# Kernel tuning notes

Hardware: AMD Instinct MI355X
Metric: run time of the kernel (lower is better)

The kernel has to match this reference:

```python
import jax, jax.numpy as jnp
import numpy as np

EMBED = 256
HEAD = 64
B, T = 16, 2048


def setup_inputs() -> dict:
    key = jax.random.key(0)
    kq, kk, kv, kwq, kwk, kwv = jax.random.split(key, 6)
    q = jax.random.normal(kq, (B, T, EMBED), dtype=jnp.float32)
    k = jax.random.normal(kk, (B, T, EMBED), dtype=jnp.float32)
    v = jax.random.normal(kv, (B, T, EMBED), dtype=jnp.float32)
    # causal mask matching the module's tril buffer semantics, broadcast over batch
    mask = jnp.tril(jnp.ones((T, T), dtype=jnp.int32))[None, :, :]
    s = 1.0 / np.sqrt(EMBED)
    Wq = (jax.random.normal(kwq, (EMBED, HEAD), dtype=jnp.float32) * s)
    Wk = (jax.random.normal(kwk, (EMBED, HEAD), dtype=jnp.float32) * s)
    Wv = (jax.random.normal(kwv, (EMBED, HEAD), dtype=jnp.float32) * s)
    return {"q": q, "k": k, "v": v, "mask": mask, "Wq": Wq, "Wk": Wk, "Wv": Wv}


def reference(q, k, v, mask, Wq, Wk, Wv):
    # projections (bias-free Linear): [B,T,E] @ [E,H] -> [B,T,H]
    C = k.shape[-1]
    qh = jnp.einsum('bte,eh->bth', q, Wq)
    kh = jnp.einsum('bte,eh->bth', k, Wk)
    vh = jnp.einsum('bte,eh->bth', v, Wv)
    # scores scaled by C**-0.5 (input embed dim, as in the source)
    wei = jnp.einsum('bth,bsh->bts', qh, kh) * (C ** -0.5)
    wei = jnp.where(mask == 0, -jnp.inf, wei)
    wei = jax.nn.softmax(wei, axis=-1)
    # dropout is identity in eval mode
    out = jnp.einsum('bts,bsh->bth', wei, vh)
    return out
```

## Files before the change

### kernel.cpp

```cpp
#include <hip/hip_runtime.h>
#include <hip/hip_bf16.h>
#include <cstdint>


#define NB 16
#define TT 2048
#define EE 256
#define HH 64

using bf16x8 = __attribute__((ext_vector_type(8))) __bf16;
using f32x4  = __attribute__((ext_vector_type(4))) float;
using u16x4  = __attribute__((ext_vector_type(4))) unsigned short;

static __device__ __forceinline__ unsigned short f2b(float f) {
  return __builtin_bit_cast(unsigned short, (__bf16)f);
}

__global__ __launch_bounds__(256) void prep_w_kernel(
    const float* __restrict__ Wq, const float* __restrict__ Wk,
    const float* __restrict__ Wv, unsigned short* __restrict__ wt) {
  int o = blockIdx.x * 256 + threadIdx.x;
  int p = o >> 14, rem = o & 16383;
  int n = rem >> 8, kk = rem & 255;
  const float* W = (p == 0) ? Wq : ((p == 1) ? Wk : Wv);
  float val = W[kk * HH + n];
  if (p == 0) val *= 0.09016844005555896f;
  wt[o] = f2b(val);
}

__global__ __launch_bounds__(256) void proj_kernel(
    const float* __restrict__ qi, const float* __restrict__ ki, const float* __restrict__ vi,
    const unsigned short* __restrict__ wt,
    unsigned short* __restrict__ qh, unsigned short* __restrict__ kh,
    unsigned short* __restrict__ vt) {
  const int p = blockIdx.y;
  const int row0 = blockIdx.x * 64;
  const float* __restrict__ src = (p == 0) ? qi : ((p == 1) ? ki : vi);
  const unsigned short* __restrict__ wp = wt + p * (HH * EE);

  __shared__ unsigned short A[64 * EE];
  const int tid = threadIdx.x;

  const float4* srcp = reinterpret_cast<const float4*>(src) + (size_t)row0 * (EE / 4);
  float4 f[16];
  #pragma unroll
  for (int i = 0; i < 16; ++i) f[i] = srcp[i * 256 + tid];
  #pragma unroll
  for (int i = 0; i < 16; ++i) {
    int c = i * 256 + tid;
    int r = c >> 6, d4 = c & 63;
    u16x4 h = { f2b(f[i].x), f2b(f[i].y), f2b(f[i].z), f2b(f[i].w) };
    int byte = r * 512 + ((d4 * 8) ^ ((r & 7) << 4));
    *reinterpret_cast<u16x4*>(reinterpret_cast<char*>(A) + byte) = h;
  }
  __syncthreads();

  const int wv = tid >> 6, lane = tid & 63, lr = lane & 15, lg = lane >> 4;
  f32x4 acc[4] = {};
  const int arow = wv * 16 + lr;
  const char* Abase = reinterpret_cast<const char*>(A) + arow * 512;
  #pragma unroll
  for (int k0 = 0; k0 < EE; k0 += 32) {
    bf16x8 af = *reinterpret_cast<const bf16x8*>(
        Abase + ((k0 * 2 + lg * 16) ^ ((arow & 7) << 4)));
    #pragma unroll
    for (int nt = 0; nt < 4; ++nt) {
      bf16x8 bfm = *reinterpret_cast<const bf16x8*>(wp + (nt * 16 + lr) * EE + k0 + lg * 8);
      acc[nt] = __builtin_amdgcn_mfma_f32_16x16x32_bf16(af, bfm, acc[nt], 0, 0, 0);
    }
  }

  if (p < 2) {
    unsigned short* dst = (p == 0) ? qh : kh;
    #pragma unroll
    for (int nt = 0; nt < 4; ++nt)
      #pragma unroll
      for (int r = 0; r < 4; ++r) {
        int grow = row0 + wv * 16 + lg * 4 + r;
        dst[(size_t)grow * HH + nt * 16 + lr] = f2b(acc[nt][r]);
      }
  } else {
    __syncthreads();
    #pragma unroll
    for (int nt = 0; nt < 4; ++nt)
      #pragma unroll
      for (int r = 0; r < 4; ++r) {
        int col = nt * 16 + lr;
        int trow = wv * 16 + lg * 4 + r;
        *reinterpret_cast<unsigned short*>(reinterpret_cast<char*>(A)
            + col * 128 + ((trow * 2) ^ ((col & 7) << 4))) = f2b(acc[nt][r]);
      }
    __syncthreads();
    const int bb = row0 >> 11, t0 = row0 & 2047;
    #pragma unroll
    for (int i = 0; i < 2; ++i) {
      int ch = i * 256 + tid;
      int col = ch >> 3, ro = (ch & 7) * 8;
      bf16x8 val = *reinterpret_cast<const bf16x8*>(reinterpret_cast<char*>(A)
          + col * 128 + ((ro * 2) ^ ((col & 7) << 4)));
      *reinterpret_cast<bf16x8*>(vt + (size_t)(bb * 64 + col) * TT + t0 + ro) = val;
    }
  }
}

__global__ __launch_bounds__(256) void attn_kernel(
    const unsigned short* __restrict__ qh, const unsigned short* __restrict__ kh,
    const unsigned short* __restrict__ vt, float* __restrict__ out) {
  __shared__ unsigned short K_lds[2][64 * 64];
  __shared__ unsigned short V_lds[2][64 * 64];
  __shared__ unsigned short P_lds[4][1024];

  const int tid = threadIdx.x;
  const int wv = tid >> 6, lane = tid & 63, lr = lane & 15, lg = lane >> 4;

  const int bid = blockIdx.x;
  const int half = bid >> 8, j = bid & 255;
  const int b = j >> 4;
  const int qt = half ? (31 - (j & 15)) : (j & 15);
  const int q0 = qt * 64;

  const unsigned short* qrow = qh + ((size_t)b * TT + q0 + wv * 16 + lr) * HH;
  bf16x8 qf0 = *reinterpret_cast<const bf16x8*>(qrow + lg * 8);
  bf16x8 qf1 = *reinterpret_cast<const bf16x8*>(qrow + 32 + lg * 8);

  const unsigned short* kb = kh + (size_t)b * TT * HH;
  const unsigned short* vb = vt + (size_t)b * HH * TT;
  char* pbase = reinterpret_cast<char*>(P_lds[wv]);

  const int rr0 = tid >> 3, of0 = (tid & 7) * 8;
  const int rr1 = (256 + tid) >> 3, of1 = (tid & 7) * 8;
  bf16x8 kr0, kr1, vr0, vr1;

#define LOADKV(kt_) do {                                                         \
    const unsigned short* kp_ = kb + (size_t)(kt_) * 64 * HH;                    \
    const unsigned short* vp_ = vb + (kt_) * 64;                                 \
    kr0 = *reinterpret_cast<const bf16x8*>(kp_ + rr0 * HH + of0);                \
    kr1 = *reinterpret_cast<const bf16x8*>(kp_ + rr1 * HH + of1);                \
    vr0 = *reinterpret_cast<const bf16x8*>(vp_ + (size_t)rr0 * TT + of0);        \
    vr1 = *reinterpret_cast<const bf16x8*>(vp_ + (size_t)rr1 * TT + of1);        \
  } while (0)

#define WRITEKV(bi_) do {                                                        \
    *reinterpret_cast<bf16x8*>(reinterpret_cast<char*>(K_lds[bi_])              \
        + rr0 * 128 + ((of0 * 2) ^ ((rr0 & 7) << 4))) = kr0;                     \
    *reinterpret_cast<bf16x8*>(reinterpret_cast<char*>(K_lds[bi_])              \
        + rr1 * 128 + ((of1 * 2) ^ ((rr1 & 7) << 4))) = kr1;                     \
    *reinterpret_cast<bf16x8*>(reinterpret_cast<char*>(V_lds[bi_])              \
        + rr0 * 128 + ((of0 * 2) ^ ((rr0 & 7) << 4))) = vr0;                     \
    *reinterpret_cast<bf16x8*>(reinterpret_cast<char*>(V_lds[bi_])              \
        + rr1 * 128 + ((of1 * 2) ^ ((rr1 & 7) << 4))) = vr1;                     \
  } while (0)

  f32x4 oa[4] = {};
  float ldacc[4] = {0.f, 0.f, 0.f, 0.f};

  LOADKV(0);
  WRITEKV(0);
  __syncthreads();

  for (int kt = 0; kt <= qt; ++kt) {
    const int cb = kt & 1;
    if (kt < qt) LOADKV(kt + 1);

    f32x4 s[4] = {};
    __builtin_amdgcn_s_setprio(1);
    #pragma unroll
    for (int ks = 0; ks < 2; ++ks)
      #pragma unroll
      for (int nt = 0; nt < 4; ++nt) {
        int key = nt * 16 + lr;
        bf16x8 kf = *reinterpret_cast<const bf16x8*>(
            reinterpret_cast<const char*>(K_lds[cb])
            + key * 128 + ((ks * 64 + lg * 16) ^ ((key & 7) << 4)));
        s[nt] = __builtin_amdgcn_mfma_f32_16x16x32_bf16(ks ? qf1 : qf0, kf, s[nt], 0, 0, 0);
      }
    __builtin_amdgcn_s_setprio(0);

    if (kt == qt) {
      #pragma unroll
      for (int nt = 0; nt < 4; ++nt)
        #pragma unroll
        for (int r = 0; r < 4; ++r)
          if (nt * 16 + lr > wv * 16 + lg * 4 + r) s[nt][r] = -__builtin_inff();
    }

    #pragma unroll
    for (int nt = 0; nt < 4; ++nt)
      #pragma unroll
      for (int r = 0; r < 4; ++r)
        s[nt][r] = exp2f(s[nt][r]);
    #pragma unroll
    for (int r = 0; r < 4; ++r)
      ldacc[r] += (s[0][r] + s[1][r]) + (s[2][r] + s[3][r]);

    #pragma unroll
    for (int nt = 0; nt < 4; ++nt)
      #pragma unroll
      for (int r = 0; r < 4; ++r) {
        int row = lg * 4 + r;
        *reinterpret_cast<unsigned short*>(pbase
            + row * 128 + (((nt * 16 + lr) * 2) ^ ((row & 7) << 4))) = f2b(s[nt][r]);
      }

    __builtin_amdgcn_s_setprio(1);
    #pragma unroll
    for (int ks = 0; ks < 2; ++ks) {
      bf16x8 pf = *reinterpret_cast<const bf16x8*>(
          pbase + lr * 128 + ((ks * 64 + lg * 16) ^ ((lr & 7) << 4)));
      #pragma unroll
      for (int nt = 0; nt < 4; ++nt) {
        int dim = nt * 16 + lr;
        bf16x8 vf = *reinterpret_cast<const bf16x8*>(
            reinterpret_cast<const char*>(V_lds[cb])
            + dim * 128 + ((ks * 64 + lg * 16) ^ ((dim & 7) << 4)));
        oa[nt] = __builtin_amdgcn_mfma_f32_16x16x32_bf16(pf, vf, oa[nt], 0, 0, 0);
      }
    }
    __builtin_amdgcn_s_setprio(0);

    if (kt < qt) WRITEKV((kt + 1) & 1);
    __syncthreads();
  }

  #pragma unroll
  for (int r = 0; r < 4; ++r) {
    float t = ldacc[r];
    t += __shfl_xor(t, 1);
    t += __shfl_xor(t, 2);
    t += __shfl_xor(t, 4);
    t += __shfl_xor(t, 8);
    float inv = 1.0f / t;
    #pragma unroll
    for (int nt = 0; nt < 4; ++nt) {
      int row = q0 + wv * 16 + lg * 4 + r;
      out[((size_t)b * TT + row) * HH + nt * 16 + lr] = oa[nt][r] * inv;
    }
  }
#undef LOADKV
#undef WRITEKV
}

extern "C" void kernel_launch(void* const* d_in, const int* in_sizes, int n_in,
                              void* d_out, int out_size, void* d_ws, size_t ws_size,
                              hipStream_t stream) {
  const float* q  = (const float*)d_in[0];
  const float* k  = (const float*)d_in[1];
  const float* v  = (const float*)d_in[2];
  const float* Wq = (const float*)d_in[4];
  const float* Wk = (const float*)d_in[5];
  const float* Wv = (const float*)d_in[6];

  char* ws = (char*)d_ws;
  unsigned short* wt = (unsigned short*)ws;
  unsigned short* qh = (unsigned short*)(ws + 98304);
  unsigned short* kh = qh + (size_t)NB * TT * HH;
  unsigned short* vt = kh + (size_t)NB * TT * HH;
  float* out = (float*)d_out;

  prep_w_kernel<<<192, 256, 0, stream>>>(Wq, Wk, Wv, wt);
  proj_kernel<<<dim3(512, 3), 256, 0, stream>>>(q, k, v, wt, qh, kh, vt);
  attn_kernel<<<512, 256, 0, stream>>>(qh, kh, vt, out);
}
```

Before: 188.7 us.

## Load projection inputs directly into MFMA registers, dropping the LDS staging tile

The projection kernel now has each wave load its fp32 input rows straight into registers in the MFMA A-fragment layout and convert them to bf16 in place. This replaces the 32KB shared-memory staging tile and its block-wide barrier. The V transpose now goes through a small per-wave LDS buffer, and launch bounds request 4 blocks per CU, aiming for higher occupancy and less LDS traffic. The trade-off is that global loads are less coalesced: each lane reads 32-byte pieces strided across rows.

```diff
diff --git a/kernel.cpp b/kernel.cpp
--- a/kernel.cpp
+++ b/kernel.cpp
@@ -15,6 +15,7 @@
 static __device__ __forceinline__ unsigned short f2b(float f) {
   return __builtin_bit_cast(unsigned short, (__bf16)f);
 }
+static __device__ __forceinline__ __bf16 f2bb(float f) { return (__bf16)f; }
 
 __global__ __launch_bounds__(256) void prep_w_kernel(
     const float* __restrict__ Wq, const float* __restrict__ Wk,
@@ -28,44 +29,39 @@
   wt[o] = f2b(val);
 }
 
-__global__ __launch_bounds__(256) void proj_kernel(
+__global__ __launch_bounds__(256, 4) void proj_kernel(
     const float* __restrict__ qi, const float* __restrict__ ki, const float* __restrict__ vi,
     const unsigned short* __restrict__ wt,
     unsigned short* __restrict__ qh, unsigned short* __restrict__ kh,
     unsigned short* __restrict__ vt) {
   const int p = blockIdx.y;
-  const int row0 = blockIdx.x * 64;
   const float* __restrict__ src = (p == 0) ? qi : ((p == 1) ? ki : vi);
   const unsigned short* __restrict__ wp = wt + p * (HH * EE);
 
-  __shared__ unsigned short A[64 * EE];
+  __shared__ unsigned short T[4][64 * 16];
+
   const int tid = threadIdx.x;
-
-  const float4* srcp = reinterpret_cast<const float4*>(src) + (size_t)row0 * (EE / 4);
-  float4 f[16];
+  const int wv = tid >> 6, lane = tid & 63, lr = lane & 15, lg = lane >> 4;
+  const int r0 = blockIdx.x * 64 + wv * 16;
+
+  const float4* ap = reinterpret_cast<const float4*>(src)
+                   + (size_t)(r0 + lr) * (EE / 4) + lg * 2;
+  float4 a[16];
   #pragma unroll
-  for (int i = 0; i < 16; ++i) f[i] = srcp[i * 256 + tid];
+  for (int i = 0; i < 8; ++i) {
+    a[2 * i]     = ap[i * 8];
+    a[2 * i + 1] = ap[i * 8 + 1];
+  }
+  __builtin_amdgcn_sched_barrier(0);
+
+  f32x4 acc[4] = {};
   #pragma unroll
-  for (int i = 0; i < 16; ++i) {
-    int c = i * 256 + tid;
-    int r = c >> 6, d4 = c & 63;
-    u16x4 h = { f2b(f[i].x), f2b(f[i].y), f2b(f[i].z), f2b(f[i].w) };
-    int byte = r * 512 + ((d4 * 8) ^ ((r & 7) << 4));
-    *reinterpret_cast<u16x4*>(reinterpret_cast<char*>(A) + byte) = h;
-  }
-  __syncthreads();
-
-  const int wv = tid >> 6, lane = tid & 63, lr = lane & 15, lg = lane >> 4;
-  f32x4 acc[4] = {};
-  const int arow = wv * 16 + lr;
-  const char* Abase = reinterpret_cast<const char*>(A) + arow * 512;
-  #pragma unroll
-  for (int k0 = 0; k0 < EE; k0 += 32) {
-    bf16x8 af = *reinterpret_cast<const bf16x8*>(
-        Abase + ((k0 * 2 + lg * 16) ^ ((arow & 7) << 4)));
+  for (int i = 0; i < 8; ++i) {
+    bf16x8 af = { f2bb(a[2*i].x),   f2bb(a[2*i].y),   f2bb(a[2*i].z),   f2bb(a[2*i].w),
+                  f2bb(a[2*i+1].x), f2bb(a[2*i+1].y), f2bb(a[2*i+1].z), f2bb(a[2*i+1].w) };
     #pragma unroll
     for (int nt = 0; nt < 4; ++nt) {
-      bf16x8 bfm = *reinterpret_cast<const bf16x8*>(wp + (nt * 16 + lr) * EE + k0 + lg * 8);
+      bf16x8 bfm = *reinterpret_cast<const bf16x8*>(wp + (nt * 16 + lr) * EE + i * 32 + lg * 8);
       acc[nt] = __builtin_amdgcn_mfma_f32_16x16x32_bf16(af, bfm, acc[nt], 0, 0, 0);
     }
   }
@@ -76,30 +72,23 @@
     for (int nt = 0; nt < 4; ++nt)
       #pragma unroll
       for (int r = 0; r < 4; ++r) {
-        int grow = row0 + wv * 16 + lg * 4 + r;
+        int grow = r0 + lg * 4 + r;
         dst[(size_t)grow * HH + nt * 16 + lr] = f2b(acc[nt][r]);
       }
   } else {
+    unsigned short* tw = T[wv];
+    #pragma unroll
+    for (int nt = 0; nt < 4; ++nt)
+      #pragma unroll
+      for (int r = 0; r < 4; ++r)
+        tw[(nt * 16 + lr) * 16 + lg * 4 + r] = f2b(acc[nt][r]);
     __syncthreads();
-    #pragma unroll
-    for (int nt = 0; nt < 4; ++nt)
-      #pragma unroll
-      for (int r = 0; r < 4; ++r) {
-        int col = nt * 16 + lr;
-        int trow = wv * 16 + lg * 4 + r;
-        *reinterpret_cast<unsigned short*>(reinterpret_cast<char*>(A)
-            + col * 128 + ((trow * 2) ^ ((col & 7) << 4))) = f2b(acc[nt][r]);
-      }
-    __syncthreads();
-    const int bb = row0 >> 11, t0 = row0 & 2047;
-    #pragma unroll
-    for (int i = 0; i < 2; ++i) {
-      int ch = i * 256 + tid;
-      int col = ch >> 3, ro = (ch & 7) * 8;
-      bf16x8 val = *reinterpret_cast<const bf16x8*>(reinterpret_cast<char*>(A)
-          + col * 128 + ((ro * 2) ^ ((col & 7) << 4)));
-      *reinterpret_cast<bf16x8*>(vt + (size_t)(bb * 64 + col) * TT + t0 + ro) = val;
-    }
+    const int bb = r0 >> 11, t0 = r0 & 2047;
+    bf16x8 v0 = *reinterpret_cast<const bf16x8*>(tw + lane * 16);
+    bf16x8 v1 = *reinterpret_cast<const bf16x8*>(tw + lane * 16 + 8);
+    unsigned short* vp = vt + (size_t)(bb * 64 + lane) * TT + t0;
+    *reinterpret_cast<bf16x8*>(vp)     = v0;
+    *reinterpret_cast<bf16x8*>(vp + 8) = v1;
   }
 }
 
```

Result: slower. 196.7 us (+4.2%).
